# Kernel optimization log

Measured on AMD Instinct MI355X. Metric: run time of the kernel, lower is better.

## Reference

```python
import jax, jax.numpy as jnp
import numpy as np

B, N, S, D1, D2 = 16, 4096, 1024, 128, 256
MLP = [256, 128]
BN_EPS = 1e-5


def setup_inputs() -> dict:
    key = jax.random.key(0)
    ks = jax.random.split(key, 12)
    inp = {
        "xyz1": jax.random.normal(ks[0], (B, 3, N), dtype=jnp.float32),
        "xyz2": jax.random.normal(ks[1], (B, 3, S), dtype=jnp.float32),
        "points1": jax.random.normal(ks[2], (B, D1, N), dtype=jnp.float32),
        "points2": jax.random.normal(ks[3], (B, D2, S), dtype=jnp.float32),
    }
    in_ch = D1 + D2  # 384
    chans = [in_ch] + MLP
    ki = 4
    for li in range(len(MLP)):
        cin, cout = chans[li], chans[li + 1]
        inp[f"w{li+1}"] = jax.random.normal(ks[ki], (cout, cin), dtype=jnp.float32) * (1.0 / np.sqrt(cin)); ki += 1
        inp[f"b{li+1}"] = jnp.zeros((cout,), dtype=jnp.float32)
        inp[f"g{li+1}"] = jnp.ones((cout,), dtype=jnp.float32)
        inp[f"beta{li+1}"] = jnp.zeros((cout,), dtype=jnp.float32)
    return inp


def _batchnorm1d(x, gamma, beta):
    # x: [B, C, N]; training-mode batch stats over (B, N)
    mean = jnp.mean(x, axis=(0, 2), keepdims=True)
    var = jnp.var(x, axis=(0, 2), keepdims=True)
    xhat = (x - mean) * jax.lax.rsqrt(var + BN_EPS)
    return xhat * gamma[None, :, None] + beta[None, :, None]


def reference(xyz1, xyz2, points1, points2, w1, b1, g1, beta1, w2, b2, g2, beta2):
    x1 = jnp.transpose(xyz1, (0, 2, 1))   # [B, N, 3]
    x2 = jnp.transpose(xyz2, (0, 2, 1))   # [B, S, 3]
    p2 = jnp.transpose(points2, (0, 2, 1))  # [B, S, D2]

    # squared pairwise distances [B, N, S]
    dists = jnp.sum((x1[:, :, None, :] - x2[:, None, :, :]) ** 2, axis=-1)
    # 3 smallest distances (original sorts then slices top-3)
    neg_d3, idx = jax.lax.top_k(-dists, 3)  # [B, N, 3]
    d3 = -neg_d3
    dist_recip = 1.0 / (d3 + 1e-8)
    weight = dist_recip / jnp.sum(dist_recip, axis=2, keepdims=True)  # [B, N, 3]

    # gather neighbor features: [B, N, 3, D2]
    feats = p2[jnp.arange(p2.shape[0])[:, None, None], idx]
    interp = jnp.sum(feats * weight[..., None], axis=2)  # [B, N, D2]

    p1 = jnp.transpose(points1, (0, 2, 1))  # [B, N, D1]
    new_points = jnp.concatenate([p1, interp], axis=-1)  # [B, N, D1+D2]
    x = jnp.transpose(new_points, (0, 2, 1))  # [B, C, N]

    for w, b, g, bt in ((w1, b1, g1, beta1), (w2, b2, g2, beta2)):
        x = jnp.einsum("oc,bcn->bon", w, x) + b[None, :, None]
        x = _batchnorm1d(x, g, bt)
        x = jax.nn.relu(x)
    return x
```

## Files before the change

kernel.cpp:

```cpp
#include <hip/hip_runtime.h>

typedef unsigned short u16;
typedef unsigned int   u32;
typedef __attribute__((ext_vector_type(8))) short bf16x8;
typedef __attribute__((ext_vector_type(8))) unsigned short u16x8;
typedef __attribute__((ext_vector_type(4))) float f32x4;

#define NB   16
#define NPTS 4096
#define SPTS 1024
#define BNT  65536

#define G2L(src, dst) __builtin_amdgcn_global_load_lds( \
    (const __attribute__((address_space(1))) void*)(src), \
    (__attribute__((address_space(3))) void*)(dst), 16, 0, 0)

__device__ __forceinline__ float bf2f(u16 u){ return __uint_as_float(((u32)u)<<16); }
__device__ __forceinline__ u16 f2bf(float f){
  u32 u = __float_as_uint(f);
  return (u16)((u + 0x7FFFu + ((u>>16)&1u))>>16);
}

__global__ __launch_bounds__(256) void convw_k(const float* __restrict__ w1, const float* __restrict__ w2,
                                               u16* __restrict__ w1b, u16* __restrict__ w2b){
  int i = blockIdx.x*256 + threadIdx.x;
  if (i < 98304) w1b[i] = f2bf(w1[i]);
  else { int j = i - 98304; w2b[j] = f2bf(w2[j]); }
}

__global__ __launch_bounds__(256) void transpose_k(const float* __restrict__ in, u16* __restrict__ out,
                                                   int C, int S, int ostride){
  __shared__ float tl[64][65];
  int t = threadIdx.x;
  int b = blockIdx.y;
  int s0 = blockIdx.x * 64;
  for (int ct = 0; ct < C; ct += 64){
    __syncthreads();
    for (int i = t; i < 4096; i += 256){
      int sl = i & 63, cl = i >> 6;
      tl[sl][cl] = in[((size_t)b*C + ct + cl)*S + s0 + sl];
    }
    __syncthreads();
    for (int i = t; i < 4096; i += 256){
      int cl = i & 63, sl = i >> 6;
      out[((size_t)b*S + s0 + sl)*ostride + ct + cl] = f2bf(tl[sl][cl]);
    }
  }
}

__global__ __launch_bounds__(512) void knn_k(const float* __restrict__ xyz1, const float* __restrict__ xyz2,
                                             const u16* __restrict__ p2t, u16* __restrict__ X){
  __shared__ float4 sxyz[SPTS];
  __shared__ float  pd[8][3][64];
  __shared__ int    pi[8][3][64];
  __shared__ float  swts[3][64];
  __shared__ int    sidx[3][64];
  int t  = threadIdx.x;
  int b  = blockIdx.x >> 6;
  int n0 = (blockIdx.x & 63) << 6;
  const float* x2b = xyz2 + (size_t)b*3*SPTS;
  for (int s = t; s < SPTS; s += 512)
    sxyz[s] = make_float4(x2b[s], x2b[SPTS+s], x2b[2*SPTS+s], 0.f);
  int q = t & 63, g = t >> 6;
  const float* x1b = xyz1 + (size_t)b*3*NPTS;
  int n = n0 + q;
  float qx = x1b[n], qy = x1b[NPTS+n], qz = x1b[2*NPTS+n];
  __syncthreads();

  float d0=3.4e38f, d1=3.4e38f, d2=3.4e38f;
  int   i0=0, i1=0, i2=0;
  int sBeg = g << 7, sEnd = sBeg + 128;
  for (int s = sBeg; s < sEnd; ++s){
    float4 p = sxyz[s];
    float dist;
    {
      #pragma clang fp contract(off)
      float dx = qx - p.x, dy = qy - p.y, dz = qz - p.z;
      dist = ((dx*dx) + (dy*dy)) + (dz*dz);
    }
    if (dist < d2){
      bool c1 = dist < d1, c0 = dist < d0;
      d2 = c1 ? d1 : dist;                 i2 = c1 ? i1 : s;
      float nd1 = c1 ? (c0 ? d0 : dist) : d1;
      int   ni1 = c1 ? (c0 ? i0 : s)    : i1;
      d0 = c0 ? dist : d0;                 i0 = c0 ? s : i0;
      d1 = nd1;                            i1 = ni1;
    }
  }
  pd[g][0][q]=d0; pd[g][1][q]=d1; pd[g][2][q]=d2;
  pi[g][0][q]=i0; pi[g][1][q]=i1; pi[g][2][q]=i2;
  __syncthreads();

  if (t < 64){
    float m0=3.4e38f, m1=3.4e38f, m2=3.4e38f;
    int   j0=0, j1=0, j2=0;
    #pragma unroll
    for (int gg = 0; gg < 8; ++gg){
      #pragma unroll
      for (int p = 0; p < 3; ++p){
        float dist = pd[gg][p][t]; int s = pi[gg][p][t];
        if (dist < m2){
          bool c1 = dist < m1, c0 = dist < m0;
          m2 = c1 ? m1 : dist;                 j2 = c1 ? j1 : s;
          float nd1 = c1 ? (c0 ? m0 : dist) : m1;
          int   ni1 = c1 ? (c0 ? j0 : s)    : j1;
          m0 = c0 ? dist : m0;                 j0 = c0 ? s : j0;
          m1 = nd1;                            j1 = ni1;
        }
      }
    }
    float r0 = 1.f/(m0 + 1e-8f), r1 = 1.f/(m1 + 1e-8f), r2 = 1.f/(m2 + 1e-8f);
    float rs = (r0 + r1) + r2;
    swts[0][t] = r0/rs; swts[1][t] = r1/rs; swts[2][t] = r2/rs;
    sidx[0][t] = j0;    sidx[1][t] = j1;    sidx[2][t] = j2;
  }
  __syncthreads();

  int w = t >> 6, lane = t & 63;
  for (int qq = w*8; qq < w*8 + 8; ++qq){
    float wa = swts[0][qq], wb = swts[1][qq], wc = swts[2][qq];
    int   j0 = sidx[0][qq], j1 = sidx[1][qq], j2 = sidx[2][qq];
    const ushort4 u0 = *(const ushort4*)(p2t + (((size_t)b*SPTS + j0)<<8) + (lane<<2));
    const ushort4 u1 = *(const ushort4*)(p2t + (((size_t)b*SPTS + j1)<<8) + (lane<<2));
    const ushort4 u2 = *(const ushort4*)(p2t + (((size_t)b*SPTS + j2)<<8) + (lane<<2));
    ushort4 ov;
    ov.x = f2bf(wa*bf2f(u0.x) + wb*bf2f(u1.x) + wc*bf2f(u2.x));
    ov.y = f2bf(wa*bf2f(u0.y) + wb*bf2f(u1.y) + wc*bf2f(u2.y));
    ov.z = f2bf(wa*bf2f(u0.z) + wb*bf2f(u1.z) + wc*bf2f(u2.z));
    ov.w = f2bf(wa*bf2f(u0.w) + wb*bf2f(u1.w) + wc*bf2f(u2.w));
    *(ushort4*)(X + ((size_t)b*NPTS + n0 + qq)*384 + 128 + (lane<<2)) = ov;
  }
}

__global__ __launch_bounds__(256) void gemm1_k(const u16* __restrict__ A, const u16* __restrict__ Bw,
                                               u16* __restrict__ Cc,
                                               float* __restrict__ psum, float* __restrict__ psq){
  const int K = 384;
  __shared__ u16 lA[64*64];
  __shared__ u16 lB[256*64];
  float* sums = (float*)lA;
  float* sqs  = sums + 256;
  int t = threadIdx.x, lane = t & 63, wid = t >> 6;
  int rowBase = blockIdx.x << 6;
  int wm = wid >> 1, wn = wid & 1;

  const char* pA[2]; int dAo[2];
  #pragma unroll
  for (int j = 0; j < 2; ++j){
    int L = j*4096 + t*16;
    int row = L >> 7, kb = L & 127;
    int kbs = kb ^ ((row & 7) << 4);
    pA[j] = (const char*)A + (size_t)(rowBase + row)*768 + kbs;
    dAo[j] = j*4096 + wid*1024;
  }
  const char* pB[8]; int dBo[8];
  #pragma unroll
  for (int j = 0; j < 8; ++j){
    int L = j*4096 + t*16;
    int row = L >> 7, kb = L & 127;
    int kbs = kb ^ ((row & 7) << 4);
    pB[j] = (const char*)Bw + (size_t)row*768 + kbs;
    dBo[j] = j*4096 + wid*1024;
  }

  f32x4 z = {0.f,0.f,0.f,0.f};
  f32x4 acc[2][8];
  #pragma unroll
  for (int m = 0; m < 2; ++m)
    #pragma unroll
    for (int n = 0; n < 8; ++n) acc[m][n] = z;

  #pragma unroll
  for (int kt = 0; kt < 6; ++kt){
    size_t ko = (size_t)kt * 128;
    #pragma unroll
    for (int j = 0; j < 2; ++j) G2L(pA[j] + ko, (char*)lA + dAo[j]);
    #pragma unroll
    for (int j = 0; j < 8; ++j) G2L(pB[j] + ko, (char*)lB + dBo[j]);
    __syncthreads();
    #pragma unroll
    for (int ks = 0; ks < 2; ++ks){
      bf16x8 af[2];
      #pragma unroll
      for (int m = 0; m < 2; ++m){
        int row = wm*32 + m*16 + (lane & 15);
        int sw = (row & 7) << 4;
        int kb = (ks*64 + ((lane >> 4) << 4)) ^ sw;
        af[m] = *(const bf16x8*)((const char*)lA + row*128 + kb);
      }
      #pragma unroll
      for (int n = 0; n < 8; ++n){
        int row = wn*128 + n*16 + (lane & 15);
        int sw = (row & 7) << 4;
        int kb = (ks*64 + ((lane >> 4) << 4)) ^ sw;
        bf16x8 bv = *(const bf16x8*)((const char*)lB + row*128 + kb);
        acc[0][n] = __builtin_amdgcn_mfma_f32_16x16x32_bf16(af[0], bv, acc[0][n], 0, 0, 0);
        acc[1][n] = __builtin_amdgcn_mfma_f32_16x16x32_bf16(af[1], bv, acc[1][n], 0, 0, 0);
      }
    }
    __syncthreads();
  }

  sums[t] = 0.f; sqs[t] = 0.f;
  __syncthreads();
  u16* bb = lB;
  int colb = wn*128 + (lane & 15);
  int rowb_l = wm*32 + ((lane >> 4) << 2);
  #pragma unroll
  for (int n = 0; n < 8; ++n){
    float s = 0.f, q = 0.f;
    #pragma unroll
    for (int m = 0; m < 2; ++m){
      #pragma unroll
      for (int r = 0; r < 4; ++r){
        float v = acc[m][n][r];
        bb[(rowb_l + m*16 + r)*256 + colb + n*16] = f2bf(v);
        s += v; q += v*v;
      }
    }
    s += __shfl_xor(s, 16); s += __shfl_xor(s, 32);
    q += __shfl_xor(q, 16); q += __shfl_xor(q, 32);
    if (lane < 16){
      atomicAdd(&sums[colb + n*16], s);
      atomicAdd(&sqs [colb + n*16], q);
    }
  }
  __syncthreads();
  psum[(size_t)blockIdx.x*256 + t] = sums[t];
  psq [(size_t)blockIdx.x*256 + t] = sqs[t];
  u16* dst = Cc + (size_t)rowBase*256;
  #pragma unroll
  for (int i = 0; i < 8; ++i)
    *(u16x8*)(dst + i*2048 + t*8) = *(const u16x8*)(bb + i*2048 + t*8);
}

__global__ __launch_bounds__(256) void gemm2_k(const u16* __restrict__ A, const u16* __restrict__ Bw,
                                               u16* __restrict__ Cc,
                                               const float* __restrict__ sc, const float* __restrict__ sh,
                                               float* __restrict__ psum, float* __restrict__ psq){
  const int K = 256, Nn = 128;
  __shared__ u16 lA[64*64];
  __shared__ u16 lB[128*64];
  __shared__ float sums[128], sqs[128];
  int t = threadIdx.x, lane = t & 63, wid = t >> 6;
  int rowBase = blockIdx.x << 6;
  int wm = wid >> 1, wn = wid & 1;

  const char* pB[4]; int dBo[4];
  #pragma unroll
  for (int j = 0; j < 4; ++j){
    int L = j*4096 + t*16;
    int row = L >> 7, kb = L & 127;
    int kbs = kb ^ ((row & 7) << 4);
    pB[j] = (const char*)Bw + ((size_t)row*K)*2 + kbs;
    dBo[j] = j*4096 + wid*1024;
  }
  int arow = t & 63, achunk = t >> 6;
  const u16* pArow = A + (size_t)(rowBase + arow)*K + achunk*16;
  int asw = (arow & 7) << 4;
  char* wA0 = (char*)lA + arow*128 + ((achunk*32)      ^ asw);
  char* wA1 = (char*)lA + arow*128 + ((achunk*32 + 16) ^ asw);

  f32x4 z = {0.f,0.f,0.f,0.f};
  f32x4 acc[2][4];
  #pragma unroll
  for (int m = 0; m < 2; ++m)
    #pragma unroll
    for (int n = 0; n < 4; ++n) acc[m][n] = z;

  for (int kk = 0; kk < K; kk += 64){
    size_t ko = (size_t)kk * 2;
    #pragma unroll
    for (int j = 0; j < 4; ++j) G2L(pB[j] + ko, (char*)lB + dBo[j]);
    u16x8 y0 = *(const u16x8*)(pArow + kk);
    u16x8 y1 = *(const u16x8*)(pArow + kk + 8);
    int k0 = kk + achunk*16;
    bf16x8 o0, o1;
    #pragma unroll
    for (int j = 0; j < 8; ++j){
      float v = bf2f((u16)y0[j]) * sc[k0 + j] + sh[k0 + j];
      o0[j] = (short)f2bf(fmaxf(v, 0.f));
    }
    #pragma unroll
    for (int j = 0; j < 8; ++j){
      float v = bf2f((u16)y1[j]) * sc[k0 + 8 + j] + sh[k0 + 8 + j];
      o1[j] = (short)f2bf(fmaxf(v, 0.f));
    }
    *(bf16x8*)wA0 = o0;
    *(bf16x8*)wA1 = o1;
    __syncthreads();
    bf16x8 af[2][2], bfv[4][2];
    #pragma unroll
    for (int m = 0; m < 2; ++m){
      int row = wm*32 + m*16 + (lane & 15);
      int sw = (row & 7) << 4;
      #pragma unroll
      for (int ks = 0; ks < 2; ++ks){
        int kb = (ks*64 + ((lane >> 4) << 4)) ^ sw;
        af[m][ks] = *(const bf16x8*)((const char*)lA + row*128 + kb);
      }
    }
    #pragma unroll
    for (int n = 0; n < 4; ++n){
      int row = wn*64 + n*16 + (lane & 15);
      int sw = (row & 7) << 4;
      #pragma unroll
      for (int ks = 0; ks < 2; ++ks){
        int kb = (ks*64 + ((lane >> 4) << 4)) ^ sw;
        bfv[n][ks] = *(const bf16x8*)((const char*)lB + row*128 + kb);
      }
    }
    #pragma unroll
    for (int ks = 0; ks < 2; ++ks)
      #pragma unroll
      for (int m = 0; m < 2; ++m)
        #pragma unroll
        for (int n = 0; n < 4; ++n)
          acc[m][n] = __builtin_amdgcn_mfma_f32_16x16x32_bf16(af[m][ks], bfv[n][ks], acc[m][n], 0, 0, 0);
    __syncthreads();
  }

  if (t < 128){ sums[t] = 0.f; sqs[t] = 0.f; }
  __syncthreads();
  int colb = wn*64 + (lane & 15);
  int rowb = rowBase + wm*32 + ((lane >> 4) << 2);
  #pragma unroll
  for (int n = 0; n < 4; ++n){
    float s = 0.f, qq2 = 0.f;
    #pragma unroll
    for (int m = 0; m < 2; ++m){
      #pragma unroll
      for (int r = 0; r < 4; ++r){
        float v = acc[m][n][r];
        Cc[(size_t)(rowb + m*16 + r)*Nn + colb + n*16] = f2bf(v);
        s += v; qq2 += v*v;
      }
    }
    atomicAdd(&sums[colb + n*16], s);
    atomicAdd(&sqs [colb + n*16], qq2);
  }
  __syncthreads();
  if (t < 128){
    psum[(size_t)blockIdx.x*128 + t] = sums[t];
    psq [(size_t)blockIdx.x*128 + t] = sqs[t];
  }
}

__global__ __launch_bounds__(256) void finalize2_k(const float* __restrict__ psum, const float* __restrict__ psq,
                                                   const float* __restrict__ g, const float* __restrict__ bet,
                                                   float* __restrict__ sc, float* __restrict__ sh,
                                                   int C, int NBLK){
  __shared__ float ls[256][8], lq[256][8];
  int c0 = blockIdx.x*8, t = threadIdx.x;
  float s[8], q[8];
  #pragma unroll
  for (int j = 0; j < 8; ++j){ s[j] = 0.f; q[j] = 0.f; }
  for (int rb = t; rb < NBLK; rb += 256){
    const float* ps = psum + (size_t)rb*C + c0;
    const float* pq = psq  + (size_t)rb*C + c0;
    #pragma unroll
    for (int j = 0; j < 8; ++j){ s[j] += ps[j]; q[j] += pq[j]; }
  }
  #pragma unroll
  for (int j = 0; j < 8; ++j){ ls[t][j] = s[j]; lq[t][j] = q[j]; }
  __syncthreads();
  for (int off = 128; off; off >>= 1){
    if (t < off){
      #pragma unroll
      for (int j = 0; j < 8; ++j){ ls[t][j] += ls[t+off][j]; lq[t][j] += lq[t+off][j]; }
    }
    __syncthreads();
  }
  if (t < 8){
    int c = c0 + t;
    const float inv = 1.f/65536.f;
    float mean = ls[0][t]*inv;
    float var  = lq[0][t]*inv - mean*mean;
    float rstd = rsqrtf(var + 1e-5f);
    float scl  = g[c]*rstd;
    sc[c] = scl;
    sh[c] = bet[c] - mean*scl;
  }
}

__global__ __launch_bounds__(256) void finalout_k(const u16* __restrict__ y2, const float* __restrict__ sc,
                                                  const float* __restrict__ sh, float* __restrict__ out){
  __shared__ float tl[128][65];
  int t  = threadIdx.x;
  int b  = blockIdx.x >> 6;
  int n0 = (blockIdx.x & 63) << 6;
  for (int i = t; i < 8192; i += 256){
    int r = i >> 7, c = i & 127;
    float v = bf2f(y2[((size_t)b*NPTS + n0 + r)*128 + c]);
    v = fmaxf(v*sc[c] + sh[c], 0.f);
    tl[c][r] = v;
  }
  __syncthreads();
  for (int i = t; i < 8192; i += 256){
    int o = i >> 6, j = i & 63;
    out[(size_t)b*128*NPTS + (size_t)o*NPTS + n0 + j] = tl[o][j];
  }
}

extern "C" void kernel_launch(void* const* d_in, const int* in_sizes, int n_in,
                              void* d_out, int out_size, void* d_ws, size_t ws_size,
                              hipStream_t stream) {
  const float* xyz1    = (const float*)d_in[0];
  const float* xyz2    = (const float*)d_in[1];
  const float* points1 = (const float*)d_in[2];
  const float* points2 = (const float*)d_in[3];
  const float* w1      = (const float*)d_in[4];
  const float* g1      = (const float*)d_in[6];
  const float* beta1   = (const float*)d_in[7];
  const float* w2      = (const float*)d_in[8];
  const float* g2      = (const float*)d_in[10];
  const float* beta2   = (const float*)d_in[11];

  char* ws = (char*)d_ws;
  u16*  X    = (u16*)ws;
  u16*  Y2   = (u16*)ws;
  u16*  Y1   = (u16*)(ws + 50331648);
  u16*  p2t  = (u16*)(ws + 83886080);
  u16*  w1b  = (u16*)(ws + 92274688);
  u16*  w2b  = (u16*)(ws + 92471296);
  float* psum1 = (float*)(ws + 83886080);
  float* psq1  = (float*)(ws + 84934656);
  float* psum2 = (float*)(ws + 85983232);
  float* psq2  = (float*)(ws + 86507520);
  float* sc1   = (float*)(ws + 87031808);
  float* sh1   = (float*)(ws + 87032832);
  float* sc2   = (float*)(ws + 87033856);
  float* sh2   = (float*)(ws + 87034368);

  convw_k<<<512, 256, 0, stream>>>(w1, w2, w1b, w2b);
  transpose_k<<<dim3(64, 16), 256, 0, stream>>>(points1, X,   128, NPTS, 384);
  transpose_k<<<dim3(16, 16), 256, 0, stream>>>(points2, p2t, 256, SPTS, 256);
  knn_k<<<1024, 512, 0, stream>>>(xyz1, xyz2, p2t, X);
  gemm1_k<<<1024, 256, 0, stream>>>(X, w1b, Y1, psum1, psq1);
  finalize2_k<<<32, 256, 0, stream>>>(psum1, psq1, g1, beta1, sc1, sh1, 256, 1024);
  gemm2_k<<<1024, 256, 0, stream>>>(Y1, w2b, Y2, sc1, sh1, psum2, psq2);
  finalize2_k<<<16, 256, 0, stream>>>(psum2, psq2, g2, beta2, sc2, sh2, 128, 1024);
  finalout_k<<<1024, 256, 0, stream>>>(Y2, sc2, sh2, (float*)d_out);
}
```

Measured before the change: 149.8 us.

## Double row tile to 128 in both MLP GEMMs and stage gemm2 output via LDS

Both GEMM kernels now process 128 rows per block instead of 64, halving the grid to 512 blocks. Each wave holds a 64x128 (gemm1) or 64x64 (gemm2) accumulator tile, so every weight tile loaded into LDS is reused across twice as many rows. gemm2 also stages its output through LDS for coalesced 16-byte stores and reduces the column statistics with shuffles before the shared atomics. The cost is more accumulator registers, lower occupancy, fewer blocks per CU, and a two-pass LDS output staging in gemm1.

```diff
diff --git a/kernel.cpp b/kernel.cpp
--- a/kernel.cpp
+++ b/kernel.cpp
@@ -135,18 +135,17 @@
 __global__ __launch_bounds__(256) void gemm1_k(const u16* __restrict__ A, const u16* __restrict__ Bw,
                                                u16* __restrict__ Cc,
                                                float* __restrict__ psum, float* __restrict__ psq){
-  const int K = 384;
-  __shared__ u16 lA[64*64];
+  __shared__ u16 lA[128*64];
   __shared__ u16 lB[256*64];
   float* sums = (float*)lA;
   float* sqs  = sums + 256;
   int t = threadIdx.x, lane = t & 63, wid = t >> 6;
-  int rowBase = blockIdx.x << 6;
+  int rowBase = blockIdx.x << 7;
   int wm = wid >> 1, wn = wid & 1;
 
-  const char* pA[2]; int dAo[2];
-  #pragma unroll
-  for (int j = 0; j < 2; ++j){
+  const char* pA[4]; int dAo[4];
+  #pragma unroll
+  for (int j = 0; j < 4; ++j){
     int L = j*4096 + t*16;
     int row = L >> 7, kb = L & 127;
     int kbs = kb ^ ((row & 7) << 4);
@@ -164,9 +163,9 @@
   }
 
   f32x4 z = {0.f,0.f,0.f,0.f};
-  f32x4 acc[2][8];
-  #pragma unroll
-  for (int m = 0; m < 2; ++m)
+  f32x4 acc[4][8];
+  #pragma unroll
+  for (int m = 0; m < 4; ++m)
     #pragma unroll
     for (int n = 0; n < 8; ++n) acc[m][n] = z;
 
@@ -174,16 +173,16 @@
   for (int kt = 0; kt < 6; ++kt){
     size_t ko = (size_t)kt * 128;
     #pragma unroll
-    for (int j = 0; j < 2; ++j) G2L(pA[j] + ko, (char*)lA + dAo[j]);
+    for (int j = 0; j < 4; ++j) G2L(pA[j] + ko, (char*)lA + dAo[j]);
     #pragma unroll
     for (int j = 0; j < 8; ++j) G2L(pB[j] + ko, (char*)lB + dBo[j]);
     __syncthreads();
     #pragma unroll
     for (int ks = 0; ks < 2; ++ks){
-      bf16x8 af[2];
-      #pragma unroll
-      for (int m = 0; m < 2; ++m){
-        int row = wm*32 + m*16 + (lane & 15);
+      bf16x8 af[4];
+      #pragma unroll
+      for (int m = 0; m < 4; ++m){
+        int row = wm*64 + m*16 + (lane & 15);
         int sw = (row & 7) << 4;
         int kb = (ks*64 + ((lane >> 4) << 4)) ^ sw;
         af[m] = *(const bf16x8*)((const char*)lA + row*128 + kb);
@@ -194,8 +193,9 @@
         int sw = (row & 7) << 4;
         int kb = (ks*64 + ((lane >> 4) << 4)) ^ sw;
         bf16x8 bv = *(const bf16x8*)((const char*)lB + row*128 + kb);
-        acc[0][n] = __builtin_amdgcn_mfma_f32_16x16x32_bf16(af[0], bv, acc[0][n], 0, 0, 0);
-        acc[1][n] = __builtin_amdgcn_mfma_f32_16x16x32_bf16(af[1], bv, acc[1][n], 0, 0, 0);
+        #pragma unroll
+        for (int m = 0; m < 4; ++m)
+          acc[m][n] = __builtin_amdgcn_mfma_f32_16x16x32_bf16(af[m], bv, acc[m][n], 0, 0, 0);
       }
     }
     __syncthreads();
@@ -203,18 +203,15 @@
 
   sums[t] = 0.f; sqs[t] = 0.f;
   __syncthreads();
-  u16* bb = lB;
   int colb = wn*128 + (lane & 15);
-  int rowb_l = wm*32 + ((lane >> 4) << 2);
   #pragma unroll
   for (int n = 0; n < 8; ++n){
     float s = 0.f, q = 0.f;
     #pragma unroll
-    for (int m = 0; m < 2; ++m){
+    for (int m = 0; m < 4; ++m){
       #pragma unroll
       for (int r = 0; r < 4; ++r){
         float v = acc[m][n][r];
-        bb[(rowb_l + m*16 + r)*256 + colb + n*16] = f2bf(v);
         s += v; q += v*v;
       }
     }
@@ -228,54 +225,74 @@
   __syncthreads();
   psum[(size_t)blockIdx.x*256 + t] = sums[t];
   psq [(size_t)blockIdx.x*256 + t] = sqs[t];
-  u16* dst = Cc + (size_t)rowBase*256;
-  #pragma unroll
-  for (int i = 0; i < 8; ++i)
-    *(u16x8*)(dst + i*2048 + t*8) = *(const u16x8*)(bb + i*2048 + t*8);
+
+  u16* bb = lB;
+  int rl0 = ((lane >> 4) << 2);
+  #pragma unroll
+  for (int h = 0; h < 2; ++h){
+    __syncthreads();
+    if (wm == h){
+      #pragma unroll
+      for (int m = 0; m < 4; ++m)
+        #pragma unroll
+        for (int n = 0; n < 8; ++n)
+          #pragma unroll
+          for (int r = 0; r < 4; ++r)
+            bb[(m*16 + rl0 + r)*256 + colb + n*16] = f2bf(acc[m][n][r]);
+    }
+    __syncthreads();
+    u16* dst = Cc + (size_t)(rowBase + h*64)*256;
+    #pragma unroll
+    for (int i = 0; i < 8; ++i)
+      *(u16x8*)(dst + i*2048 + t*8) = *(const u16x8*)(bb + i*2048 + t*8);
+  }
 }
 
 __global__ __launch_bounds__(256) void gemm2_k(const u16* __restrict__ A, const u16* __restrict__ Bw,
                                                u16* __restrict__ Cc,
                                                const float* __restrict__ sc, const float* __restrict__ sh,
                                                float* __restrict__ psum, float* __restrict__ psq){
-  const int K = 256, Nn = 128;
-  __shared__ u16 lA[64*64];
-  __shared__ u16 lB[128*64];
+  const int K = 256;
+  __shared__ u16 L[16384];
   __shared__ float sums[128], sqs[128];
   int t = threadIdx.x, lane = t & 63, wid = t >> 6;
-  int rowBase = blockIdx.x << 6;
+  int rowBase = blockIdx.x << 7;
   int wm = wid >> 1, wn = wid & 1;
 
   const char* pB[4]; int dBo[4];
   #pragma unroll
   for (int j = 0; j < 4; ++j){
-    int L = j*4096 + t*16;
-    int row = L >> 7, kb = L & 127;
+    int Lo = j*4096 + t*16;
+    int row = Lo >> 7, kb = Lo & 127;
     int kbs = kb ^ ((row & 7) << 4);
     pB[j] = (const char*)Bw + ((size_t)row*K)*2 + kbs;
-    dBo[j] = j*4096 + wid*1024;
-  }
-  int arow = t & 63, achunk = t >> 6;
-  const u16* pArow = A + (size_t)(rowBase + arow)*K + achunk*16;
+    dBo[j] = 16384 + j*4096 + wid*1024;
+  }
+  int arow = t & 127, h = t >> 7;
+  const u16* pArow = A + (size_t)(rowBase + arow)*K + h*32;
   int asw = (arow & 7) << 4;
-  char* wA0 = (char*)lA + arow*128 + ((achunk*32)      ^ asw);
-  char* wA1 = (char*)lA + arow*128 + ((achunk*32 + 16) ^ asw);
+  int wAo0 = arow*128 + ((h*64      ) ^ asw);
+  int wAo1 = arow*128 + ((h*64 + 16 ) ^ asw);
+  int wAo2 = arow*128 + ((h*64 + 32 ) ^ asw);
+  int wAo3 = arow*128 + ((h*64 + 48 ) ^ asw);
 
   f32x4 z = {0.f,0.f,0.f,0.f};
-  f32x4 acc[2][4];
-  #pragma unroll
-  for (int m = 0; m < 2; ++m)
+  f32x4 acc[4][4];
+  #pragma unroll
+  for (int m = 0; m < 4; ++m)
     #pragma unroll
     for (int n = 0; n < 4; ++n) acc[m][n] = z;
 
   for (int kk = 0; kk < K; kk += 64){
     size_t ko = (size_t)kk * 2;
     #pragma unroll
-    for (int j = 0; j < 4; ++j) G2L(pB[j] + ko, (char*)lB + dBo[j]);
+    for (int j = 0; j < 4; ++j) G2L(pB[j] + ko, (char*)L + dBo[j]);
     u16x8 y0 = *(const u16x8*)(pArow + kk);
     u16x8 y1 = *(const u16x8*)(pArow + kk + 8);
-    int k0 = kk + achunk*16;
-    bf16x8 o0, o1;
+    u16x8 y2 = *(const u16x8*)(pArow + kk + 16);
+    u16x8 y3 = *(const u16x8*)(pArow + kk + 24);
+    int k0 = kk + h*32;
+    bf16x8 o0, o1, o2, o3;
     #pragma unroll
     for (int j = 0; j < 8; ++j){
       float v = bf2f((u16)y0[j]) * sc[k0 + j] + sh[k0 + j];
@@ -286,64 +303,77 @@
       float v = bf2f((u16)y1[j]) * sc[k0 + 8 + j] + sh[k0 + 8 + j];
       o1[j] = (short)f2bf(fmaxf(v, 0.f));
     }
-    *(bf16x8*)wA0 = o0;
-    *(bf16x8*)wA1 = o1;
-    __syncthreads();
-    bf16x8 af[2][2], bfv[4][2];
-    #pragma unroll
-    for (int m = 0; m < 2; ++m){
-      int row = wm*32 + m*16 + (lane & 15);
-      int sw = (row & 7) << 4;
-      #pragma unroll
-      for (int ks = 0; ks < 2; ++ks){
+    #pragma unroll
+    for (int j = 0; j < 8; ++j){
+      float v = bf2f((u16)y2[j]) * sc[k0 + 16 + j] + sh[k0 + 16 + j];
+      o2[j] = (short)f2bf(fmaxf(v, 0.f));
+    }
+    #pragma unroll
+    for (int j = 0; j < 8; ++j){
+      float v = bf2f((u16)y3[j]) * sc[k0 + 24 + j] + sh[k0 + 24 + j];
+      o3[j] = (short)f2bf(fmaxf(v, 0.f));
+    }
+    *(bf16x8*)((char*)L + wAo0) = o0;
+    *(bf16x8*)((char*)L + wAo1) = o1;
+    *(bf16x8*)((char*)L + wAo2) = o2;
+    *(bf16x8*)((char*)L + wAo3) = o3;
+    __syncthreads();
+    #pragma unroll
+    for (int ks = 0; ks < 2; ++ks){
+      bf16x8 af[4];
+      #pragma unroll
+      for (int m = 0; m < 4; ++m){
+        int row = wm*64 + m*16 + (lane & 15);
+        int sw = (row & 7) << 4;
         int kb = (ks*64 + ((lane >> 4) << 4)) ^ sw;
-        af[m][ks] = *(const bf16x8*)((const char*)lA + row*128 + kb);
-      }
-    }
-    #pragma unroll
-    for (int n = 0; n < 4; ++n){
-      int row = wn*64 + n*16 + (lane & 15);
-      int sw = (row & 7) << 4;
-      #pragma unroll
-      for (int ks = 0; ks < 2; ++ks){
+        af[m] = *(const bf16x8*)((const char*)L + row*128 + kb);
+      }
+      #pragma unroll
+      for (int n = 0; n < 4; ++n){
+        int row = wn*64 + n*16 + (lane & 15);
+        int sw = (row & 7) << 4;
         int kb = (ks*64 + ((lane >> 4) << 4)) ^ sw;
-        bfv[n][ks] = *(const bf16x8*)((const char*)lB + row*128 + kb);
-      }
-    }
-    #pragma unroll
-    for (int ks = 0; ks < 2; ++ks)
-      #pragma unroll
-      for (int m = 0; m < 2; ++m)
+        bf16x8 bv = *(const bf16x8*)((const char*)L + 16384 + row*128 + kb);
         #pragma unroll
-        for (int n = 0; n < 4; ++n)
-          acc[m][n] = __builtin_amdgcn_mfma_f32_16x16x32_bf16(af[m][ks], bfv[n][ks], acc[m][n], 0, 0, 0);
+        for (int m = 0; m < 4; ++m)
+          acc[m][n] = __builtin_amdgcn_mfma_f32_16x16x32_bf16(af[m], bv, acc[m][n], 0, 0, 0);
+      }
+    }
     __syncthreads();
   }
 
   if (t < 128){ sums[t] = 0.f; sqs[t] = 0.f; }
   __syncthreads();
   int colb = wn*64 + (lane & 15);
-  int rowb = rowBase + wm*32 + ((lane >> 4) << 2);
+  int rl0 = ((lane >> 4) << 2);
   #pragma unroll
   for (int n = 0; n < 4; ++n){
-    float s = 0.f, qq2 = 0.f;
-    #pragma unroll
-    for (int m = 0; m < 2; ++m){
+    float s = 0.f, q = 0.f;
+    #pragma unroll
+    for (int m = 0; m < 4; ++m){
       #pragma unroll
       for (int r = 0; r < 4; ++r){
         float v = acc[m][n][r];
-        Cc[(size_t)(rowb + m*16 + r)*Nn + colb + n*16] = f2bf(v);
-        s += v; qq2 += v*v;
-      }
-    }
-    atomicAdd(&sums[colb + n*16], s);
-    atomicAdd(&sqs [colb + n*16], qq2);
+        L[(wm*64 + m*16 + rl0 + r)*128 + colb + n*16] = f2bf(v);
+        s += v; q += v*v;
+      }
+    }
+    s += __shfl_xor(s, 16); s += __shfl_xor(s, 32);
+    q += __shfl_xor(q, 16); q += __shfl_xor(q, 32);
+    if (lane < 16){
+      atomicAdd(&sums[colb + n*16], s);
+      atomicAdd(&sqs [colb + n*16], q);
+    }
   }
   __syncthreads();
   if (t < 128){
     psum[(size_t)blockIdx.x*128 + t] = sums[t];
     psq [(size_t)blockIdx.x*128 + t] = sqs[t];
   }
+  u16* dst = Cc + (size_t)rowBase*128;
+  #pragma unroll
+  for (int i = 0; i < 8; ++i)
+    *(u16x8*)(dst + i*2048 + t*8) = *(const u16x8*)(L + i*2048 + t*8);
 }
 
 __global__ __launch_bounds__(256) void finalize2_k(const float* __restrict__ psum, const float* __restrict__ psq,
@@ -436,9 +466,9 @@
   transpose_k<<<dim3(64, 16), 256, 0, stream>>>(points1, X,   128, NPTS, 384);
   transpose_k<<<dim3(16, 16), 256, 0, stream>>>(points2, p2t, 256, SPTS, 256);
   knn_k<<<1024, 512, 0, stream>>>(xyz1, xyz2, p2t, X);
-  gemm1_k<<<1024, 256, 0, stream>>>(X, w1b, Y1, psum1, psq1);
-  finalize2_k<<<32, 256, 0, stream>>>(psum1, psq1, g1, beta1, sc1, sh1, 256, 1024);
-  gemm2_k<<<1024, 256, 0, stream>>>(Y1, w2b, Y2, sc1, sh1, psum2, psq2);
-  finalize2_k<<<16, 256, 0, stream>>>(psum2, psq2, g2, beta2, sc2, sh2, 128, 1024);
+  gemm1_k<<<512, 256, 0, stream>>>(X, w1b, Y1, psum1, psq1);
+  finalize2_k<<<32, 256, 0, stream>>>(psum1, psq1, g1, beta1, sc1, sh1, 256, 512);
+  gemm2_k<<<512, 256, 0, stream>>>(Y1, w2b, Y2, sc1, sh1, psum2, psq2);
+  finalize2_k<<<16, 256, 0, stream>>>(psum2, psq2, g2, beta2, sc2, sh2, 128, 512);
   finalout_k<<<1024, 256, 0, stream>>>(Y2, sc2, sh2, (float*)d_out);
 }
```

After: 144.4 us (median of 2 runs). 3.6% less time.
